# Performance work log

Hardware: AMD Instinct MI355X
Metric: run time of the kernel (lower is better)

The kernel has to match this reference:

```python
import jax, jax.numpy as jnp
import numpy as np

B, L, K = 16, 512, 30          # proteins, residues per protein, kNN neighbors
N = B * L
H, FC = 32, 3                  # h_channels, frame_channels
C = H + FC                     # fused sphere channels (35)
HEADS, AC, VC = 8, 16, 8       # heads, alpha channels (H//2), value channels (H//4)
RBF_N, POS_N = 16, 16
EF = RBF_N + POS_N

# idealized backbone atom positions (N, CA, C) in the local residue frame
IDEAL_BB = np.array([[-0.525, 1.363, 0.0], [0.0, 0.0, 0.0], [1.526, 0.0, 0.0]], dtype=np.float32)
# cartesian (x,y,z) -> real-SH l=1 ordering (y,z,x)
P_SH = np.array([[0., 1., 0.], [0., 0., 1.], [1., 0., 0.]], dtype=np.float32)


def _knn_edges(trans):
    # per-chain brute-force kNN (chains are contiguous blocks of length L)
    X = trans.reshape(B, L, 3)
    d2 = jnp.sum((X[:, :, None, :] - X[:, None, :, :]) ** 2, axis=-1)  # [B,L,L]
    d2 = d2 + jnp.eye(L, dtype=d2.dtype) * 1e9                          # exclude self
    _, idx = jax.lax.top_k(-d2, K)                                      # [B,L,K]
    off = (jnp.arange(B) * L)[:, None, None]
    src = (idx + off).reshape(-1)              # neighbor (edge_index[0])
    tgt = jnp.repeat(jnp.arange(N), K)         # center   (edge_index[1])
    return src, tgt


def _edge_rot_mat(vec):
    # rotation aligning the edge vector with the y axis (eSCN init_edge_rot_mat style)
    nx = vec / (jnp.linalg.norm(vec, axis=-1, keepdims=True) + 1e-12)
    ref = jnp.where(jnp.abs(nx[:, :1]) < 0.9,
                    jnp.array([1., 0., 0.], dtype=vec.dtype),
                    jnp.array([0., 0., 1.], dtype=vec.dtype))
    nz = jnp.cross(nx, ref)
    nz = nz / (jnp.linalg.norm(nz, axis=-1, keepdims=True) + 1e-12)
    ny = jnp.cross(nx, nz)
    ny = ny / (jnp.linalg.norm(ny, axis=-1, keepdims=True) + 1e-12)
    return jnp.stack([nz, nx, ny], axis=-2)  # [E,3,3]


def _rbf(d, d_min=0.0, d_max=20.0, count=RBF_N):
    mu = jnp.linspace(d_min, d_max, count)
    sigma = (d_max - d_min) / count
    return jnp.exp(-(((d[:, None] - mu) / sigma) ** 2))


def _pos_emb(src, tgt, num=POS_N):
    d = (src - tgt).astype(jnp.float32)
    freq = jnp.exp(jnp.arange(0, num, 2, dtype=jnp.float32) * (-np.log(10000.0) / num))
    ang = d[:, None] * freq
    return jnp.concatenate([jnp.cos(ang), jnp.sin(ang)], axis=-1)


def _forward(rots, trans, node_emb, batch, x_mask, noising_mask,
             W_alpha, a_vec, W_v, W_o, W_g, W_2):
    src, tgt = _knn_edges(trans)
    vec = trans[src] - trans[tgt]
    dist = jnp.linalg.norm(vec, axis=-1)
    valid = jnp.isfinite(dist) & (dist > 1e-3)  # edge_select, applied as mask

    R = _edge_rot_mat(vec)
    P = jnp.asarray(P_SH)
    D1 = jnp.einsum('ij,ejk,lk->eil', P, R, P)  # l=1 Wigner in real-SH basis [E,3,3]

    edge_features = jnp.concatenate([_rbf(dist), _pos_emb(src, tgt)], axis=-1)  # [E,32]

    # fuse node features with backbone frame atoms and editability flag
    frame_atoms = jnp.einsum('nij,aj->nai', rots, jnp.asarray(IDEAL_BB))  # [N,3atoms,3xyz]
    editable = noising_mask & (~x_mask)
    emb = jnp.zeros((N, 4, C), dtype=node_emb.dtype)
    emb = emb.at[:, :, :H].set(node_emb)
    emb = emb.at[:, 1:4, H:].set(jnp.swapaxes(frame_atoms, -1, -2))
    emb = emb.at[:, 0, C - 1].set(editable.astype(node_emb.dtype))

    # gather + rotate source features into edge frames
    xs = emb[src]                                                   # [E,4,C]
    xs_rot = jnp.concatenate([xs[:, :1], jnp.einsum('eij,ejc->eic', D1, xs[:, 1:])], axis=1)

    # invariant attention logits (l=0 of rotated src, l=0 of tgt, edge feats)
    inv = jnp.concatenate([xs_rot[:, 0], emb[tgt, 0], edge_features], axis=-1)  # [E,102]
    hdn = jax.nn.silu(inv @ W_alpha).reshape(-1, HEADS, AC)
    logits = jax.nn.leaky_relu(jnp.einsum('ehk,hk->eh', hdn, a_vec), 0.2)
    logits = jnp.where(valid[:, None], logits, -1e9)

    # segment softmax over incoming edges of each target node
    mx = jax.lax.stop_gradient(jax.ops.segment_max(logits, tgt, num_segments=N))
    ex = jnp.exp(logits - mx[tgt]) * valid[:, None].astype(logits.dtype)
    den = jax.ops.segment_sum(ex, tgt, num_segments=N)
    alpha = ex / (den[tgt] + 1e-9)                                  # [E,HEADS]

    # equivariant values, attention-weighted, rotate back, scatter
    v = (xs_rot @ W_v).reshape(-1, 4, HEADS, VC)
    m = (v * alpha[:, None, :, None]).reshape(-1, 4, HEADS * VC)
    m = jnp.concatenate([m[:, :1], jnp.einsum('eji,ejc->eic', D1, m[:, 1:])], axis=1)  # D^T
    agg = jax.ops.segment_sum(m, tgt, num_segments=N)               # [N,4,64]

    y = agg @ W_o                                                    # [N,4,H]
    gate = jax.nn.silu(y[:, 0] @ W_g)                                # invariant gating FFN
    return (y * gate[:, None, :]) @ W_2                              # [N,4,H]


def setup_inputs():
    key = jax.random.key(0)
    ks = jax.random.split(key, 12)
    rots = jax.vmap(lambda m: jnp.linalg.qr(m)[0])(jax.random.normal(ks[0], (N, 3, 3)))
    trans = jax.random.normal(ks[1], (N, 3)) * 10.0
    node_emb = jax.random.normal(ks[2], (N, 4, H))
    batch = jnp.repeat(jnp.arange(B, dtype=jnp.int32), L)
    x_mask = jax.random.randint(ks[3], (N,), 0, 2).astype(bool)
    noising_mask = jax.random.randint(ks[4], (N,), 0, 2).astype(bool)
    s = lambda k, sh, fan: jax.random.normal(k, sh) / np.sqrt(fan)
    return dict(rots=rots, trans=trans, node_emb=node_emb, batch=batch,
                x_mask=x_mask, noising_mask=noising_mask,
                W_alpha=s(ks[5], (2 * C + EF, HEADS * AC), 2 * C + EF),
                a_vec=s(ks[6], (HEADS, AC), AC),
                W_v=s(ks[7], (C, HEADS * VC), C),
                W_o=s(ks[8], (HEADS * VC, H), HEADS * VC),
                W_g=s(ks[9], (H, H), H),
                W_2=s(ks[10], (H, H), H))


def reference(rots, trans, node_emb, batch, x_mask, noising_mask,
              W_alpha, a_vec, W_v, W_o, W_g, W_2):
    return _forward(rots, trans, node_emb, batch, x_mask, noising_mask,
                    W_alpha, a_vec, W_v, W_o, W_g, W_2)
```

## Files before the change

### kernel.cpp

```cpp
#include <hip/hip_runtime.h>
#include <cstdint>

#define B_ 16
#define L_ 512
#define N_ 8192
#define K_ 30
#define E_ (N_*K_)
#define H_ 32
#define C_ 35

typedef uint16_t u16;
typedef uint32_t u32;
typedef unsigned long long u64;

static __device__ __forceinline__ float ldf(const void* p, int i, int bf) {
    return bf ? __uint_as_float(((u32)((const u16*)p)[i]) << 16)
              : ((const float*)p)[i];
}
static __device__ __forceinline__ int ldmask(const void* p, int i, int mode) {
    if (mode == 0) return ((const unsigned char*)p)[i] != 0;
    if (mode == 2) return ((const u32*)p)[2*i] != 0;
    return ((const u32*)p)[i] != 0;
}
static __device__ __forceinline__ u16 f2bf(float f) {
    u32 x = __float_as_uint(f);
    u32 r = x + 0x7FFFu + ((x >> 16) & 1u);
    return (u16)(r >> 16);
}
static __device__ __forceinline__ float fsilu(float x) {
    return x * __builtin_amdgcn_rcpf(1.f + __expf(-x));
}

__global__ void detect_kernel(const u16* __restrict__ tr, const u32* __restrict__ xm,
                              int* __restrict__ flag)
{
    int lane = threadIdx.x;
    int cnt = 0;
    for (int i = lane; i < 256; i += 64) {
        u16 v = tr[2 * i];
        int e = (v >> 7) & 0xFF;
        if ((e >= 100 && e <= 141) || (v & 0x7FFFu) == 0) cnt++;
    }
    int anyBig = 0, oddNZ = 0;
    for (int i = lane; i < 1024; i += 64) {
        u32 w = xm[i];
        if (w & ~1u) anyBig = 1;
        if ((i & 1) && w) oddNZ = 1;
    }
    #pragma unroll
    for (int d = 1; d < 64; d <<= 1) {
        cnt    += __shfl_xor(cnt, d, 64);
        anyBig |= __shfl_xor(anyBig, d, 64);
        oddNZ  |= __shfl_xor(oddNZ, d, 64);
    }
    if (lane == 0) {
        flag[0] = (cnt >= 192) ? 1 : 0;
        flag[1] = anyBig ? 0 : (oddNZ ? 1 : 2);
    }
}

#define U_TRANS 24576
#define U_WA    37632
#define U_AV    37760
#define U_WV    40000
#define U_WO    42048
#define U_WG    43072
#define U_W2    44096

__global__ void conv_kernel(const void* trans,
                            const void* Wa, const void* av, const void* Wv,
                            const void* Wo, const void* Wg, const void* W2,
                            const int* __restrict__ flag,
                            float* c_trans, float* c_Wa, float* c_av, float* c_Wv,
                            float* c_Wo, float* c_Wg, float* c_W2)
{
    int gid = blockIdx.x * 256 + threadIdx.x;
    if (gid >= U_W2) return;
    int bf = flag[0];
    if      (gid < U_TRANS) c_trans[gid]           = ldf(trans, gid,           bf);
    else if (gid < U_WA)    c_Wa   [gid - U_TRANS] = ldf(Wa,    gid - U_TRANS, bf);
    else if (gid < U_AV)    c_av   [gid - U_WA]    = ldf(av,    gid - U_WA,    bf);
    else if (gid < U_WV)    c_Wv   [gid - U_AV]    = ldf(Wv,    gid - U_AV,    bf);
    else if (gid < U_WO)    c_Wo   [gid - U_WV]    = ldf(Wo,    gid - U_WV,    bf);
    else if (gid < U_WG)    c_Wg   [gid - U_WO]    = ldf(Wg,    gid - U_WO,    bf);
    else                    c_W2   [gid - U_WG]    = ldf(W2,    gid - U_WG,    bf);
}

#define DPP_MIN_STEP(CTRL) \
    { u32 olo = (u32)__builtin_amdgcn_update_dpp((int)lo, (int)lo, CTRL, 0xF, 0xF, false); \
      u32 ohi = (u32)__builtin_amdgcn_update_dpp((int)hi, (int)hi, CTRL, 0xF, 0xF, false); \
      u64 o = (((u64)ohi) << 32) | olo; \
      if (o < m) m = o; \
      lo = (u32)m; hi = (u32)(m >> 32); }

__global__ __launch_bounds__(256) void knn_kernel(const float* __restrict__ trans,
                                                  int* __restrict__ srcArr)
{
    __shared__ float xs[L_], ys[L_], zs[L_];
    const int tid  = threadIdx.x;
    const int t0   = blockIdx.x * 4;
    const int base = (t0 >> 9) << 9;

    for (int i = tid; i < L_; i += 256) {
        xs[i] = trans[(base + i) * 3 + 0];
        ys[i] = trans[(base + i) * 3 + 1];
        zs[i] = trans[(base + i) * 3 + 2];
    }
    __syncthreads();

    const int wid = tid >> 6, lane = tid & 63;
    const int t = t0 + wid;
    const int l = t & 511;
    const float tx = xs[l], ty = ys[l], tz = zs[l];

    u64 key[8];
    #pragma unroll
    for (int i = 0; i < 8; ++i) {
        int j = lane + (i << 6);
        float dx = __fsub_rn(tx, xs[j]);
        float dy = __fsub_rn(ty, ys[j]);
        float dz = __fsub_rn(tz, zs[j]);
        float d2 = __fadd_rn(__fadd_rn(__fmul_rn(dx, dx), __fmul_rn(dy, dy)), __fmul_rn(dz, dz));
        if (j == l) d2 = __fadd_rn(d2, 1e9f);
        key[i] = (((u64)__float_as_uint(d2)) << 32) | (u32)j;
    }

    int myres = 0;
    for (int k = 0; k < K_; ++k) {
        u64 m = key[0];
        #pragma unroll
        for (int i = 1; i < 8; ++i)
            if (key[i] < m) m = key[i];
        u32 lo = (u32)m, hi = (u32)(m >> 32);
        DPP_MIN_STEP(0x111)
        DPP_MIN_STEP(0x112)
        DPP_MIN_STEP(0x114)
        DPP_MIN_STEP(0x118)
        DPP_MIN_STEP(0x142)
        DPP_MIN_STEP(0x143)
        u32 glo = (u32)__builtin_amdgcn_readlane((int)lo, 63);
        u32 ghi = (u32)__builtin_amdgcn_readlane((int)hi, 63);
        u64 gm = (((u64)ghi) << 32) | glo;
        if (lane == k) myres = (int)(glo & 511u);
        #pragma unroll
        for (int i = 0; i < 8; ++i)
            if (key[i] == gm) key[i] = ~0ULL;
    }
    if (lane < K_) srcArr[t * K_ + lane] = base + myres;
}

__constant__ float cBB[9] = {-0.525f, 1.363f, 0.f,  0.f, 0.f, 0.f,  1.526f, 0.f, 0.f};

__global__ __launch_bounds__(256) void node_kernel(
    const void* __restrict__ rots, const void* __restrict__ node,
    const void* __restrict__ xm, const void* __restrict__ nm,
    const int* __restrict__ flag,
    const float* __restrict__ Wa, const float* __restrict__ Wv,
    float* __restrict__ hsrc, float* __restrict__ htgt,
    float* __restrict__ ptab, float* __restrict__ V)
{
    const int bid = blockIdx.x, tid = threadIdx.x;
    if (bid >= N_) {
        int d = bid - N_;
        if (tid < 128) {
            float dd = (float)(d - 512);
            float acc = 0.f;
            #pragma unroll
            for (int q = 0; q < 8; ++q) {
                float fr = expf((float)(2 * q) * (-0.5756462732485115f));
                float ang = dd * fr;
                acc = fmaf(cosf(ang), Wa[(86 + q) * 128 + tid], acc);
                acc = fmaf(sinf(ang), Wa[(94 + q) * 128 + tid], acc);
            }
            ptab[(size_t)d * 128 + tid] = acc;
        }
        return;
    }
    __shared__ float e[140];
    const int bf = flag[0], mm = flag[1];
    if (tid < 140) {
        int r = tid / 35, c = tid - r * 35;
        float v;
        if (c < H_) {
            v = ldf(node, bid * 128 + r * 32 + c, bf);
        } else if (r == 0) {
            v = (c == 34) ? ((ldmask(nm, bid, mm) && !ldmask(xm, bid, mm)) ? 1.f : 0.f) : 0.f;
        } else {
            int i = r - 1, a = c - 32;
            v = ldf(rots, bid*9 + i*3 + 0, bf) * cBB[a*3 + 0]
              + ldf(rots, bid*9 + i*3 + 1, bf) * cBB[a*3 + 1]
              + ldf(rots, bid*9 + i*3 + 2, bf) * cBB[a*3 + 2];
        }
        e[tid] = v;
    }
    __syncthreads();
    if (tid < 128) {
        float a = 0.f, b = 0.f;
        #pragma unroll 5
        for (int i = 0; i < 35; ++i) {
            float v = e[i];
            a = fmaf(v, Wa[i * 128 + tid],        a);
            b = fmaf(v, Wa[(35 + i) * 128 + tid], b);
        }
        hsrc[(size_t)bid * 128 + tid] = a;
        htgt[(size_t)bid * 128 + tid] = b;
    }
    {
        int r = tid >> 6, cc = tid & 63;
        const float* er = e + r * 35;
        float acc = 0.f;
        #pragma unroll 5
        for (int cp = 0; cp < 35; ++cp) acc = fmaf(er[cp], Wv[cp * 64 + cc], acc);
        V[(size_t)bid * 256 + tid] = acc;
    }
}

__global__ __launch_bounds__(128) void logits_kernel(
    const float* __restrict__ trans, const int* __restrict__ srcArr,
    const float* __restrict__ hsrc, const float* __restrict__ htgt,
    const float* __restrict__ ptab, const float* __restrict__ Wa,
    const float* __restrict__ avec, float* __restrict__ logitsw)
{
    __shared__ float rbfS[2][32][20];
    __shared__ int   srcS[2][32];
    __shared__ int   tgtS[2][32];
    __shared__ int   dS[2][32];
    __shared__ float lgS[2][256];
    const int tid = threadIdx.x, wid = tid >> 6, lane = tid & 63;

    float2 wrb[16];
    #pragma unroll
    for (int j = 0; j < 16; ++j)
        wrb[j] = ((const float2*)(Wa + (70 + j) * 128))[lane];
    const float2 av = ((const float2*)avec)[lane];

    const int e0 = (blockIdx.x * 2 + wid) * 32;

    {
        const int el  = lane & 31;
        const int e   = e0 + el;
        const int tgt = e / K_;
        int src = srcArr[e];
        src = (src < 0) ? 0 : ((src >= N_) ? (N_ - 1) : src);
        float vx = trans[src*3+0] - trans[tgt*3+0];
        float vy = trans[src*3+1] - trans[tgt*3+1];
        float vz = trans[src*3+2] - trans[tgt*3+2];
        float dist = sqrtf(vx*vx + vy*vy + vz*vz);
        bool valid = isfinite(dist) && (dist > 1e-3f);
        int d = src - tgt + 512;
        d = (d < 0) ? 0 : ((d > 1023) ? 1023 : d);
        if (lane < 32) {
            srcS[wid][el] = src;
            tgtS[wid][el] = tgt;
            dS[wid][el]   = d | (valid ? 0 : (1 << 16));
        }
        const int jb = (lane >> 5) * 8;
        #pragma unroll
        for (int j = 0; j < 8; ++j) {
            float tt = (dist - (float)(jb + j) * (20.f/15.f)) * 0.8f;
            rbfS[wid][el][jb + j] = __expf(-tt * tt);
        }
    }
    __syncthreads();

    #pragma unroll 2
    for (int q = 0; q < 32; ++q) {
        const int src = srcS[wid][q];
        const int tgt = tgtS[wid][q];
        const int dm  = dS[wid][q];
        const int d   = dm & 0xFFFF;
        const bool valid = (dm >> 16) == 0;

        float2 hs = ((const float2*)(hsrc + (size_t)src * 128))[lane];
        float2 ht = ((const float2*)(htgt + (size_t)tgt * 128))[lane];
        float2 pt = ((const float2*)(ptab + (size_t)d   * 128))[lane];
        float acc0 = hs.x + ht.x + pt.x;
        float acc1 = hs.y + ht.y + pt.y;
        const float4* rp = (const float4*)(&rbfS[wid][q][0]);
        #pragma unroll
        for (int jj = 0; jj < 4; ++jj) {
            float4 rb = rp[jj];
            acc0 = fmaf(rb.x, wrb[4*jj+0].x, acc0); acc1 = fmaf(rb.x, wrb[4*jj+0].y, acc1);
            acc0 = fmaf(rb.y, wrb[4*jj+1].x, acc0); acc1 = fmaf(rb.y, wrb[4*jj+1].y, acc1);
            acc0 = fmaf(rb.z, wrb[4*jj+2].x, acc0); acc1 = fmaf(rb.z, wrb[4*jj+2].y, acc1);
            acc0 = fmaf(rb.w, wrb[4*jj+3].x, acc0); acc1 = fmaf(rb.w, wrb[4*jj+3].y, acc1);
        }
        float part = fsilu(acc0) * av.x + fsilu(acc1) * av.y;
        #pragma unroll
        for (int s = 1; s < 8; s <<= 1) part += __shfl_xor(part, s, 64);
        float lg = (part >= 0.f) ? part : 0.2f * part;
        if (!valid) lg = -1e9f;
        lg = (fabsf(lg) < 1e30f) ? lg : -1e9f;
        if ((lane & 7) == 0) lgS[wid][q * 8 + (lane >> 3)] = lg;
    }
    __syncthreads();
    {
        float4* dst = (float4*)(logitsw + (size_t)e0 * 8);
        dst[lane] = ((const float4*)lgS[wid])[lane];
    }
}

__global__ __launch_bounds__(256) void agg_out_kernel(
    const float* __restrict__ V, const int* __restrict__ srcArr,
    const float* __restrict__ logitsw,
    const float* __restrict__ Wo, const float* __restrict__ Wg,
    const float* __restrict__ W2,
    const int* __restrict__ flag, void* __restrict__ outv)
{
    __shared__ int   srcs[K_];
    __shared__ float aggS[256];
    __shared__ float ybuf[128];
    __shared__ float gbuf[32];
    const int bid = blockIdx.x;
    const int t   = ((bid & 7) << 10) | (bid >> 3);
    const int tid = threadIdx.x;
    const int obf = flag[0];
    const int cc = tid & 63, r = tid >> 6, h = cc >> 3;

    if (tid < K_) {
        int s = srcArr[t * K_ + tid];
        srcs[tid] = (s < 0) ? 0 : ((s >= N_) ? (N_ - 1) : s);
    }

    const float* lp = logitsw + (size_t)t * 240 + h;
    float lg[K_];
    float mx = -1e30f;
    #pragma unroll
    for (int k = 0; k < K_; ++k) { lg[k] = lp[k * 8]; mx = fmaxf(mx, lg[k]); }
    float den = 0.f;
    #pragma unroll
    for (int k = 0; k < K_; ++k) {
        float e = (lg[k] > -1e8f) ? __expf(lg[k] - mx) : 0.f;
        lg[k] = e; den += e;
    }
    const float inv = 1.f / (den + 1e-9f);
    __syncthreads();

    const int off = (r << 6) | cc;
    float acc = 0.f;
    #pragma unroll 6
    for (int k = 0; k < K_; ++k)
        acc = fmaf(lg[k], V[(size_t)srcs[k] * 256 + off], acc);
    aggS[tid] = acc * inv;
    __syncthreads();

    if (tid < 128) {
        int rr = tid >> 5, o = tid & 31;
        float y = 0.f;
        #pragma unroll
        for (int c = 0; c < 64; ++c) y = fmaf(aggS[rr * 64 + c], Wo[c * 32 + o], y);
        ybuf[tid] = y;
    }
    __syncthreads();
    if (tid < 32) {
        float g = 0.f;
        #pragma unroll
        for (int o = 0; o < 32; ++o) g = fmaf(ybuf[o], Wg[o * 32 + tid], g);
        gbuf[tid] = g / (1.f + expf(-g));
    }
    __syncthreads();
    if (tid < 128) {
        int rr = tid >> 5, hh = tid & 31;
        float o = 0.f;
        #pragma unroll
        for (int g = 0; g < 32; ++g) o = fmaf(ybuf[rr * 32 + g] * gbuf[g], W2[g * 32 + hh], o);
        o = (fabsf(o) < 1e30f) ? o : 0.f;
        size_t idx = (size_t)t * 128 + tid;
        if (obf) ((u16*)outv)[idx] = f2bf(o);
        else     ((float*)outv)[idx] = o;
    }
}

extern "C" void kernel_launch(void* const* d_in, const int* in_sizes, int n_in,
                              void* d_out, int out_size, void* d_ws, size_t ws_size,
                              hipStream_t stream)
{
    const void* rots         = d_in[0];
    const void* trans        = d_in[1];
    const void* node_emb     = d_in[2];
    const void* x_mask       = d_in[4];
    const void* noising_mask = d_in[5];
    const void* Wa           = d_in[6];
    const void* avec         = d_in[7];
    const void* Wv           = d_in[8];
    const void* Wo           = d_in[9];
    const void* Wg           = d_in[10];
    const void* W2           = d_in[11];

    char* ws = (char*)d_ws;
    int*   flag    = (int*)  (ws + 0);
    float* c_trans = (float*)(ws + 64);
    float* c_Wa    = (float*)(ws + 98368);
    float* c_av    = (float*)(ws + 150592);
    float* c_Wv    = (float*)(ws + 151104);
    float* c_Wo    = (float*)(ws + 160064);
    float* c_Wg    = (float*)(ws + 168256);
    float* c_W2    = (float*)(ws + 172352);
    int*   srcArr  = (int*)  (ws + 176448);
    float* hsrc    = (float*)(ws + 1159488);
    float* htgt    = (float*)(ws + 5353792);
    float* ptab    = (float*)(ws + 9548096);
    float* logitsw = (float*)(ws + 10072384);
    float* V       = (float*)(ws + 17936704);

    hipLaunchKernelGGL(detect_kernel, dim3(1), dim3(64), 0, stream,
                       (const u16*)trans, (const u32*)x_mask, flag);
    hipLaunchKernelGGL(conv_kernel, dim3((U_W2 + 255) / 256), dim3(256), 0, stream,
                       trans, Wa, avec, Wv, Wo, Wg, W2, flag,
                       c_trans, c_Wa, c_av, c_Wv, c_Wo, c_Wg, c_W2);
    hipLaunchKernelGGL(knn_kernel,  dim3(N_/4),     dim3(256), 0, stream, c_trans, srcArr);
    hipLaunchKernelGGL(node_kernel, dim3(N_+1024),  dim3(256), 0, stream,
                       rots, node_emb, x_mask, noising_mask, flag, c_Wa, c_Wv,
                       hsrc, htgt, ptab, V);
    hipLaunchKernelGGL(logits_kernel, dim3(E_/64),  dim3(128), 0, stream,
                       c_trans, srcArr, hsrc, htgt, ptab, c_Wa, c_av, logitsw);
    hipLaunchKernelGGL(agg_out_kernel, dim3(N_),    dim3(256), 0, stream,
                       V, srcArr, logitsw, c_Wo, c_Wg, c_W2, flag, d_out);
}
```

Before: 227.1 us.

## Merge prep kernels into one launch and fuse logits with aggregation

Replaces the six-kernel pipeline with two launches. The detect, convert, kNN, node-projection and position-table stages now run as block ranges of a single kernel, and each block re-detects the dtype flag itself. The edge-logit computation is fused into the per-node aggregation kernel, so the logits buffer is no longer written to and read back from global memory. This removes launch gaps and a full-size intermediate round trip, at the cost of redundant dtype detection in every block and a single-node granularity for the logit work.

New measurement: 224.3 us. Within noise of the previous version (-1.2%).

```diff
diff --git a/kernel.cpp b/kernel.cpp
--- a/kernel.cpp
+++ b/kernel.cpp
@@ -17,6 +17,9 @@
     return bf ? __uint_as_float(((u32)((const u16*)p)[i]) << 16)
               : ((const float*)p)[i];
 }
+static __device__ __forceinline__ float bfu16(u16 x) {
+    return __uint_as_float(((u32)x) << 16);
+}
 static __device__ __forceinline__ int ldmask(const void* p, int i, int mode) {
     if (mode == 0) return ((const unsigned char*)p)[i] != 0;
     if (mode == 2) return ((const u32*)p)[2*i] != 0;
@@ -31,16 +34,20 @@
     return x * __builtin_amdgcn_rcpf(1.f + __expf(-x));
 }
 
-__global__ void detect_kernel(const u16* __restrict__ tr, const u32* __restrict__ xm,
-                              int* __restrict__ flag)
-{
-    int lane = threadIdx.x;
+static __device__ __forceinline__ int detect_bf(const void* tr, int lane) {
+    const u16* p = (const u16*)tr;
     int cnt = 0;
     for (int i = lane; i < 256; i += 64) {
-        u16 v = tr[2 * i];
+        u16 v = p[2 * i];
         int e = (v >> 7) & 0xFF;
         if ((e >= 100 && e <= 141) || (v & 0x7FFFu) == 0) cnt++;
     }
+    #pragma unroll
+    for (int d = 1; d < 64; d <<= 1) cnt += __shfl_xor(cnt, d, 64);
+    return cnt >= 192;
+}
+static __device__ __forceinline__ int detect_mm(const void* xmv, int lane) {
+    const u32* xm = (const u32*)xmv;
     int anyBig = 0, oddNZ = 0;
     for (int i = lane; i < 1024; i += 64) {
         u32 w = xm[i];
@@ -49,42 +56,13 @@
     }
     #pragma unroll
     for (int d = 1; d < 64; d <<= 1) {
-        cnt    += __shfl_xor(cnt, d, 64);
         anyBig |= __shfl_xor(anyBig, d, 64);
         oddNZ  |= __shfl_xor(oddNZ, d, 64);
     }
-    if (lane == 0) {
-        flag[0] = (cnt >= 192) ? 1 : 0;
-        flag[1] = anyBig ? 0 : (oddNZ ? 1 : 2);
-    }
-}
-
-#define U_TRANS 24576
-#define U_WA    37632
-#define U_AV    37760
-#define U_WV    40000
-#define U_WO    42048
-#define U_WG    43072
-#define U_W2    44096
-
-__global__ void conv_kernel(const void* trans,
-                            const void* Wa, const void* av, const void* Wv,
-                            const void* Wo, const void* Wg, const void* W2,
-                            const int* __restrict__ flag,
-                            float* c_trans, float* c_Wa, float* c_av, float* c_Wv,
-                            float* c_Wo, float* c_Wg, float* c_W2)
-{
-    int gid = blockIdx.x * 256 + threadIdx.x;
-    if (gid >= U_W2) return;
-    int bf = flag[0];
-    if      (gid < U_TRANS) c_trans[gid]           = ldf(trans, gid,           bf);
-    else if (gid < U_WA)    c_Wa   [gid - U_TRANS] = ldf(Wa,    gid - U_TRANS, bf);
-    else if (gid < U_AV)    c_av   [gid - U_WA]    = ldf(av,    gid - U_WA,    bf);
-    else if (gid < U_WV)    c_Wv   [gid - U_AV]    = ldf(Wv,    gid - U_AV,    bf);
-    else if (gid < U_WO)    c_Wo   [gid - U_WV]    = ldf(Wo,    gid - U_WV,    bf);
-    else if (gid < U_WG)    c_Wg   [gid - U_WO]    = ldf(Wg,    gid - U_WO,    bf);
-    else                    c_W2   [gid - U_WG]    = ldf(W2,    gid - U_WG,    bf);
-}
+    return anyBig ? 0 : (oddNZ ? 1 : 2);
+}
+
+__constant__ float cBB[9] = {-0.525f, 1.363f, 0.f,  0.f, 0.f, 0.f,  1.526f, 0.f, 0.f};
 
 #define DPP_MIN_STEP(CTRL) \
     { u32 olo = (u32)__builtin_amdgcn_update_dpp((int)lo, (int)lo, CTRL, 0xF, 0xF, false); \
@@ -93,255 +71,310 @@
       if (o < m) m = o; \
       lo = (u32)m; hi = (u32)(m >> 32); }
 
-__global__ __launch_bounds__(256) void knn_kernel(const float* __restrict__ trans,
-                                                  int* __restrict__ srcArr)
+__global__ __launch_bounds__(256) void mega_kernel(
+    const void* __restrict__ rots, const void* __restrict__ trans,
+    const void* __restrict__ node, const void* __restrict__ xm,
+    const void* __restrict__ nm,
+    const void* __restrict__ Wa, const void* __restrict__ av,
+    const void* __restrict__ Wv, const void* __restrict__ Wo,
+    const void* __restrict__ Wg, const void* __restrict__ W2,
+    int* __restrict__ flag, int* __restrict__ srcArr,
+    float* __restrict__ hsrc, float* __restrict__ htgt,
+    float* __restrict__ ptab, float* __restrict__ V,
+    float* __restrict__ c_wrb, float* __restrict__ c_av,
+    float* __restrict__ c_Wo, float* __restrict__ c_Wg, float* __restrict__ c_W2)
 {
-    __shared__ float xs[L_], ys[L_], zs[L_];
-    const int tid  = threadIdx.x;
-    const int t0   = blockIdx.x * 4;
-    const int base = (t0 >> 9) << 9;
-
-    for (int i = tid; i < L_; i += 256) {
-        xs[i] = trans[(base + i) * 3 + 0];
-        ys[i] = trans[(base + i) * 3 + 1];
-        zs[i] = trans[(base + i) * 3 + 2];
-    }
-    __syncthreads();
-
-    const int wid = tid >> 6, lane = tid & 63;
-    const int t = t0 + wid;
-    const int l = t & 511;
-    const float tx = xs[l], ty = ys[l], tz = zs[l];
-
-    u64 key[8];
-    #pragma unroll
-    for (int i = 0; i < 8; ++i) {
-        int j = lane + (i << 6);
-        float dx = __fsub_rn(tx, xs[j]);
-        float dy = __fsub_rn(ty, ys[j]);
-        float dz = __fsub_rn(tz, zs[j]);
-        float d2 = __fadd_rn(__fadd_rn(__fmul_rn(dx, dx), __fmul_rn(dy, dy)), __fmul_rn(dz, dz));
-        if (j == l) d2 = __fadd_rn(d2, 1e9f);
-        key[i] = (((u64)__float_as_uint(d2)) << 32) | (u32)j;
-    }
-
-    int myres = 0;
-    for (int k = 0; k < K_; ++k) {
-        u64 m = key[0];
-        #pragma unroll
-        for (int i = 1; i < 8; ++i)
-            if (key[i] < m) m = key[i];
-        u32 lo = (u32)m, hi = (u32)(m >> 32);
-        DPP_MIN_STEP(0x111)
-        DPP_MIN_STEP(0x112)
-        DPP_MIN_STEP(0x114)
-        DPP_MIN_STEP(0x118)
-        DPP_MIN_STEP(0x142)
-        DPP_MIN_STEP(0x143)
-        u32 glo = (u32)__builtin_amdgcn_readlane((int)lo, 63);
-        u32 ghi = (u32)__builtin_amdgcn_readlane((int)hi, 63);
-        u64 gm = (((u64)ghi) << 32) | glo;
-        if (lane == k) myres = (int)(glo & 511u);
-        #pragma unroll
-        for (int i = 0; i < 8; ++i)
-            if (key[i] == gm) key[i] = ~0ULL;
-    }
-    if (lane < K_) srcArr[t * K_ + lane] = base + myres;
-}
-
-__constant__ float cBB[9] = {-0.525f, 1.363f, 0.f,  0.f, 0.f, 0.f,  1.526f, 0.f, 0.f};
-
-__global__ __launch_bounds__(256) void node_kernel(
-    const void* __restrict__ rots, const void* __restrict__ node,
-    const void* __restrict__ xm, const void* __restrict__ nm,
-    const int* __restrict__ flag,
-    const float* __restrict__ Wa, const float* __restrict__ Wv,
-    float* __restrict__ hsrc, float* __restrict__ htgt,
-    float* __restrict__ ptab, float* __restrict__ V)
-{
+    __shared__ float sX[L_], sY[L_], sZ[L_];
+    __shared__ float eS[140];
+    __shared__ int flagS[2];
     const int bid = blockIdx.x, tid = threadIdx.x;
-    if (bid >= N_) {
-        int d = bid - N_;
+    const int lane = tid & 63, wid = tid >> 6;
+
+    if (bid < 2048) {
+        if (wid == 0) {
+            int bf = detect_bf(trans, lane);
+            if (lane == 0) flagS[0] = bf;
+        }
+        __syncthreads();
+        const int bf = flagS[0];
+        const int t0 = bid * 4;
+        const int base = (t0 >> 9) << 9;
+        if (bf) {
+            const u16* tp = (const u16*)trans;
+            for (int i = tid; i < L_; i += 256) {
+                sX[i] = bfu16(tp[(base + i) * 3 + 0]);
+                sY[i] = bfu16(tp[(base + i) * 3 + 1]);
+                sZ[i] = bfu16(tp[(base + i) * 3 + 2]);
+            }
+        } else {
+            const float* tp = (const float*)trans;
+            for (int i = tid; i < L_; i += 256) {
+                sX[i] = tp[(base + i) * 3 + 0];
+                sY[i] = tp[(base + i) * 3 + 1];
+                sZ[i] = tp[(base + i) * 3 + 2];
+            }
+        }
+        __syncthreads();
+
+        const int t = t0 + wid;
+        const int l = t & 511;
+        const float tx = sX[l], ty = sY[l], tz = sZ[l];
+
+        u64 key[8];
+        #pragma unroll
+        for (int i = 0; i < 8; ++i) {
+            int j = lane + (i << 6);
+            float dx = __fsub_rn(tx, sX[j]);
+            float dy = __fsub_rn(ty, sY[j]);
+            float dz = __fsub_rn(tz, sZ[j]);
+            float d2 = __fadd_rn(__fadd_rn(__fmul_rn(dx, dx), __fmul_rn(dy, dy)), __fmul_rn(dz, dz));
+            if (j == l) d2 = __fadd_rn(d2, 1e9f);
+            key[i] = (((u64)__float_as_uint(d2)) << 32) | (u32)j;
+        }
+        int myres = 0;
+        for (int k = 0; k < K_; ++k) {
+            u64 m = key[0];
+            #pragma unroll
+            for (int i = 1; i < 8; ++i)
+                if (key[i] < m) m = key[i];
+            u32 lo = (u32)m, hi = (u32)(m >> 32);
+            DPP_MIN_STEP(0x111)
+            DPP_MIN_STEP(0x112)
+            DPP_MIN_STEP(0x114)
+            DPP_MIN_STEP(0x118)
+            DPP_MIN_STEP(0x142)
+            DPP_MIN_STEP(0x143)
+            u32 glo = (u32)__builtin_amdgcn_readlane((int)lo, 63);
+            u32 ghi = (u32)__builtin_amdgcn_readlane((int)hi, 63);
+            u64 gm = (((u64)ghi) << 32) | glo;
+            if (lane == k) myres = (int)(glo & 511u);
+            #pragma unroll
+            for (int i = 0; i < 8; ++i)
+                if (key[i] == gm) key[i] = ~0ULL;
+        }
+        if (lane < K_) srcArr[t * K_ + lane] = base + myres;
+
+    } else if (bid < 10240) {
+        const int n = bid - 2048;
+        if (wid == 0) {
+            int bf = detect_bf(trans, lane);
+            int mm = detect_mm(xm, lane);
+            if (lane == 0) { flagS[0] = bf; flagS[1] = mm; }
+        }
+        __syncthreads();
+        const int bf = flagS[0], mm = flagS[1];
+        if (tid < 140) {
+            int r = tid / 35, c = tid - r * 35;
+            float v;
+            if (c < H_) {
+                v = ldf(node, n * 128 + r * 32 + c, bf);
+            } else if (r == 0) {
+                v = (c == 34) ? ((ldmask(nm, n, mm) && !ldmask(xm, n, mm)) ? 1.f : 0.f) : 0.f;
+            } else {
+                int i = r - 1, a = c - 32;
+                v = ldf(rots, n*9 + i*3 + 0, bf) * cBB[a*3 + 0]
+                  + ldf(rots, n*9 + i*3 + 1, bf) * cBB[a*3 + 1]
+                  + ldf(rots, n*9 + i*3 + 2, bf) * cBB[a*3 + 2];
+            }
+            eS[tid] = v;
+        }
+        __syncthreads();
+        const int r = tid >> 6, cc = tid & 63;
+        if (bf) {
+            const u16* wa = (const u16*)Wa;
+            const u16* wv = (const u16*)Wv;
+            if (tid < 128) {
+                float a = 0.f, b = 0.f;
+                #pragma unroll 5
+                for (int i = 0; i < 35; ++i) {
+                    float v = eS[i];
+                    a = fmaf(v, bfu16(wa[i * 128 + tid]),        a);
+                    b = fmaf(v, bfu16(wa[(35 + i) * 128 + tid]), b);
+                }
+                hsrc[(size_t)n * 128 + tid] = a;
+                htgt[(size_t)n * 128 + tid] = b;
+            }
+            const float* er = eS + r * 35;
+            float acc = 0.f;
+            #pragma unroll 5
+            for (int cp = 0; cp < 35; ++cp) acc = fmaf(er[cp], bfu16(wv[cp * 64 + cc]), acc);
+            V[(size_t)n * 256 + tid] = acc;
+        } else {
+            const float* wa = (const float*)Wa;
+            const float* wv = (const float*)Wv;
+            if (tid < 128) {
+                float a = 0.f, b = 0.f;
+                #pragma unroll 5
+                for (int i = 0; i < 35; ++i) {
+                    float v = eS[i];
+                    a = fmaf(v, wa[i * 128 + tid],        a);
+                    b = fmaf(v, wa[(35 + i) * 128 + tid], b);
+                }
+                hsrc[(size_t)n * 128 + tid] = a;
+                htgt[(size_t)n * 128 + tid] = b;
+            }
+            const float* er = eS + r * 35;
+            float acc = 0.f;
+            #pragma unroll 5
+            for (int cp = 0; cp < 35; ++cp) acc = fmaf(er[cp], wv[cp * 64 + cc], acc);
+            V[(size_t)n * 256 + tid] = acc;
+        }
+
+    } else if (bid < 11264) {
+        const int d = bid - 10240;
+        if (wid == 0) {
+            int bf = detect_bf(trans, lane);
+            if (lane == 0) flagS[0] = bf;
+        }
+        __syncthreads();
+        const int bf = flagS[0];
         if (tid < 128) {
             float dd = (float)(d - 512);
             float acc = 0.f;
-            #pragma unroll
-            for (int q = 0; q < 8; ++q) {
-                float fr = expf((float)(2 * q) * (-0.5756462732485115f));
-                float ang = dd * fr;
-                acc = fmaf(cosf(ang), Wa[(86 + q) * 128 + tid], acc);
-                acc = fmaf(sinf(ang), Wa[(94 + q) * 128 + tid], acc);
+            if (bf) {
+                const u16* wa = (const u16*)Wa;
+                #pragma unroll
+                for (int q = 0; q < 8; ++q) {
+                    float fr = expf((float)(2 * q) * (-0.5756462732485115f));
+                    float ang = dd * fr;
+                    acc = fmaf(cosf(ang), bfu16(wa[(86 + q) * 128 + tid]), acc);
+                    acc = fmaf(sinf(ang), bfu16(wa[(94 + q) * 128 + tid]), acc);
+                }
+            } else {
+                const float* wa = (const float*)Wa;
+                #pragma unroll
+                for (int q = 0; q < 8; ++q) {
+                    float fr = expf((float)(2 * q) * (-0.5756462732485115f));
+                    float ang = dd * fr;
+                    acc = fmaf(cosf(ang), wa[(86 + q) * 128 + tid], acc);
+                    acc = fmaf(sinf(ang), wa[(94 + q) * 128 + tid], acc);
+                }
             }
             ptab[(size_t)d * 128 + tid] = acc;
         }
-        return;
-    }
-    __shared__ float e[140];
-    const int bf = flag[0], mm = flag[1];
-    if (tid < 140) {
-        int r = tid / 35, c = tid - r * 35;
-        float v;
-        if (c < H_) {
-            v = ldf(node, bid * 128 + r * 32 + c, bf);
-        } else if (r == 0) {
-            v = (c == 34) ? ((ldmask(nm, bid, mm) && !ldmask(xm, bid, mm)) ? 1.f : 0.f) : 0.f;
-        } else {
-            int i = r - 1, a = c - 32;
-            v = ldf(rots, bid*9 + i*3 + 0, bf) * cBB[a*3 + 0]
-              + ldf(rots, bid*9 + i*3 + 1, bf) * cBB[a*3 + 1]
-              + ldf(rots, bid*9 + i*3 + 2, bf) * cBB[a*3 + 2];
-        }
-        e[tid] = v;
-    }
-    __syncthreads();
-    if (tid < 128) {
-        float a = 0.f, b = 0.f;
-        #pragma unroll 5
-        for (int i = 0; i < 35; ++i) {
-            float v = e[i];
-            a = fmaf(v, Wa[i * 128 + tid],        a);
-            b = fmaf(v, Wa[(35 + i) * 128 + tid], b);
-        }
-        hsrc[(size_t)bid * 128 + tid] = a;
-        htgt[(size_t)bid * 128 + tid] = b;
-    }
-    {
-        int r = tid >> 6, cc = tid & 63;
-        const float* er = e + r * 35;
-        float acc = 0.f;
-        #pragma unroll 5
-        for (int cp = 0; cp < 35; ++cp) acc = fmaf(er[cp], Wv[cp * 64 + cc], acc);
-        V[(size_t)bid * 256 + tid] = acc;
-    }
-}
-
-__global__ __launch_bounds__(128) void logits_kernel(
-    const float* __restrict__ trans, const int* __restrict__ srcArr,
+
+    } else {
+        if (wid == 0) {
+            int bf = detect_bf(trans, lane);
+            if (lane == 0) flagS[0] = bf;
+        }
+        __syncthreads();
+        const int bf = flagS[0];
+        if (bid == 11264 && tid == 0) flag[0] = bf;
+        int g0 = (bid - 11264) * 256 + tid;
+        for (int i = g0; i < 6272; i += 2048) {
+            if      (i < 2048) c_wrb[i]        = ldf(Wa, 70 * 128 + i, bf);
+            else if (i < 2176) c_av[i - 2048]  = ldf(av, i - 2048, bf);
+            else if (i < 4224) c_Wo[i - 2176]  = ldf(Wo, i - 2176, bf);
+            else if (i < 5248) c_Wg[i - 4224]  = ldf(Wg, i - 4224, bf);
+            else               c_W2[i - 5248]  = ldf(W2, i - 5248, bf);
+        }
+    }
+}
+
+__global__ __launch_bounds__(256) void edge_agg_kernel(
+    const void* __restrict__ trans, const int* __restrict__ srcArr,
     const float* __restrict__ hsrc, const float* __restrict__ htgt,
-    const float* __restrict__ ptab, const float* __restrict__ Wa,
-    const float* __restrict__ avec, float* __restrict__ logitsw)
-{
-    __shared__ float rbfS[2][32][20];
-    __shared__ int   srcS[2][32];
-    __shared__ int   tgtS[2][32];
-    __shared__ int   dS[2][32];
-    __shared__ float lgS[2][256];
-    const int tid = threadIdx.x, wid = tid >> 6, lane = tid & 63;
-
-    float2 wrb[16];
-    #pragma unroll
-    for (int j = 0; j < 16; ++j)
-        wrb[j] = ((const float2*)(Wa + (70 + j) * 128))[lane];
-    const float2 av = ((const float2*)avec)[lane];
-
-    const int e0 = (blockIdx.x * 2 + wid) * 32;
-
-    {
-        const int el  = lane & 31;
-        const int e   = e0 + el;
-        const int tgt = e / K_;
-        int src = srcArr[e];
-        src = (src < 0) ? 0 : ((src >= N_) ? (N_ - 1) : src);
-        float vx = trans[src*3+0] - trans[tgt*3+0];
-        float vy = trans[src*3+1] - trans[tgt*3+1];
-        float vz = trans[src*3+2] - trans[tgt*3+2];
-        float dist = sqrtf(vx*vx + vy*vy + vz*vz);
-        bool valid = isfinite(dist) && (dist > 1e-3f);
-        int d = src - tgt + 512;
-        d = (d < 0) ? 0 : ((d > 1023) ? 1023 : d);
-        if (lane < 32) {
-            srcS[wid][el] = src;
-            tgtS[wid][el] = tgt;
-            dS[wid][el]   = d | (valid ? 0 : (1 << 16));
-        }
-        const int jb = (lane >> 5) * 8;
-        #pragma unroll
-        for (int j = 0; j < 8; ++j) {
-            float tt = (dist - (float)(jb + j) * (20.f/15.f)) * 0.8f;
-            rbfS[wid][el][jb + j] = __expf(-tt * tt);
-        }
-    }
-    __syncthreads();
-
-    #pragma unroll 2
-    for (int q = 0; q < 32; ++q) {
-        const int src = srcS[wid][q];
-        const int tgt = tgtS[wid][q];
-        const int dm  = dS[wid][q];
-        const int d   = dm & 0xFFFF;
-        const bool valid = (dm >> 16) == 0;
-
-        float2 hs = ((const float2*)(hsrc + (size_t)src * 128))[lane];
-        float2 ht = ((const float2*)(htgt + (size_t)tgt * 128))[lane];
-        float2 pt = ((const float2*)(ptab + (size_t)d   * 128))[lane];
-        float acc0 = hs.x + ht.x + pt.x;
-        float acc1 = hs.y + ht.y + pt.y;
-        const float4* rp = (const float4*)(&rbfS[wid][q][0]);
-        #pragma unroll
-        for (int jj = 0; jj < 4; ++jj) {
-            float4 rb = rp[jj];
-            acc0 = fmaf(rb.x, wrb[4*jj+0].x, acc0); acc1 = fmaf(rb.x, wrb[4*jj+0].y, acc1);
-            acc0 = fmaf(rb.y, wrb[4*jj+1].x, acc0); acc1 = fmaf(rb.y, wrb[4*jj+1].y, acc1);
-            acc0 = fmaf(rb.z, wrb[4*jj+2].x, acc0); acc1 = fmaf(rb.z, wrb[4*jj+2].y, acc1);
-            acc0 = fmaf(rb.w, wrb[4*jj+3].x, acc0); acc1 = fmaf(rb.w, wrb[4*jj+3].y, acc1);
-        }
-        float part = fsilu(acc0) * av.x + fsilu(acc1) * av.y;
-        #pragma unroll
-        for (int s = 1; s < 8; s <<= 1) part += __shfl_xor(part, s, 64);
-        float lg = (part >= 0.f) ? part : 0.2f * part;
-        if (!valid) lg = -1e9f;
-        lg = (fabsf(lg) < 1e30f) ? lg : -1e9f;
-        if ((lane & 7) == 0) lgS[wid][q * 8 + (lane >> 3)] = lg;
-    }
-    __syncthreads();
-    {
-        float4* dst = (float4*)(logitsw + (size_t)e0 * 8);
-        dst[lane] = ((const float4*)lgS[wid])[lane];
-    }
-}
-
-__global__ __launch_bounds__(256) void agg_out_kernel(
-    const float* __restrict__ V, const int* __restrict__ srcArr,
-    const float* __restrict__ logitsw,
+    const float* __restrict__ ptab, const float* __restrict__ V,
+    const float* __restrict__ c_wrb, const float* __restrict__ c_av,
     const float* __restrict__ Wo, const float* __restrict__ Wg,
     const float* __restrict__ W2,
     const int* __restrict__ flag, void* __restrict__ outv)
 {
-    __shared__ int   srcs[K_];
+    __shared__ float rbfS[K_][20];
+    __shared__ int   srcS[K_];
+    __shared__ int   dS[K_];
+    __shared__ float lgS[240];
     __shared__ float aggS[256];
     __shared__ float ybuf[128];
     __shared__ float gbuf[32];
-    const int bid = blockIdx.x;
+    const int bid = blockIdx.x, tid = threadIdx.x;
     const int t   = ((bid & 7) << 10) | (bid >> 3);
-    const int tid = threadIdx.x;
-    const int obf = flag[0];
-    const int cc = tid & 63, r = tid >> 6, h = cc >> 3;
-
-    if (tid < K_) {
-        int s = srcArr[t * K_ + tid];
-        srcs[tid] = (s < 0) ? 0 : ((s >= N_) ? (N_ - 1) : s);
-    }
-
-    const float* lp = logitsw + (size_t)t * 240 + h;
-    float lg[K_];
-    float mx = -1e30f;
+    const int lane = tid & 63, wid = tid >> 6;
+    const int bf = flag[0];
+
+    float2 wrb[16];
     #pragma unroll
-    for (int k = 0; k < K_; ++k) { lg[k] = lp[k * 8]; mx = fmaxf(mx, lg[k]); }
-    float den = 0.f;
+    for (int j = 0; j < 16; ++j) wrb[j] = ((const float2*)c_wrb)[j * 64 + lane];
+    const float2 avv = ((const float2*)c_av)[lane];
+
+    if (tid < 2 * K_) {
+        const int k = tid >> 1, half = tid & 1;
+        const int e = t * K_ + k;
+        int src = srcArr[e];
+        src = (src < 0) ? 0 : ((src >= N_) ? (N_ - 1) : src);
+        float vx = ldf(trans, src*3+0, bf) - ldf(trans, t*3+0, bf);
+        float vy = ldf(trans, src*3+1, bf) - ldf(trans, t*3+1, bf);
+        float vz = ldf(trans, src*3+2, bf) - ldf(trans, t*3+2, bf);
+        float dist = sqrtf(vx*vx + vy*vy + vz*vz);
+        bool valid = isfinite(dist) && (dist > 1e-3f);
+        int d = src - t + 512;
+        d = (d < 0) ? 0 : ((d > 1023) ? 1023 : d);
+        if (half == 0) {
+            srcS[k] = src;
+            dS[k]   = d | (valid ? 0 : (1 << 16));
+        }
+        const int jb = half * 8;
+        #pragma unroll
+        for (int j = 0; j < 8; ++j) {
+            float tt = (dist - (float)(jb + j) * (20.f/15.f)) * 0.8f;
+            rbfS[k][jb + j] = __expf(-tt * tt);
+        }
+    }
+    __syncthreads();
+
+    const float2 htv = ((const float2*)(htgt + (size_t)t * 128))[lane];
     #pragma unroll
-    for (int k = 0; k < K_; ++k) {
-        float e = (lg[k] > -1e8f) ? __expf(lg[k] - mx) : 0.f;
-        lg[k] = e; den += e;
-    }
-    const float inv = 1.f / (den + 1e-9f);
+    for (int j = 0; j < 8; ++j) {
+        const int k = wid * 8 + j;
+        if (k < K_) {
+            const int src = srcS[k];
+            const int dm  = dS[k];
+            const int d   = dm & 0xFFFF;
+            const bool valid = (dm >> 16) == 0;
+            float2 hs = ((const float2*)(hsrc + (size_t)src * 128))[lane];
+            float2 pt = ((const float2*)(ptab + (size_t)d   * 128))[lane];
+            float acc0 = hs.x + htv.x + pt.x;
+            float acc1 = hs.y + htv.y + pt.y;
+            const float4* rp = (const float4*)(&rbfS[k][0]);
+            #pragma unroll
+            for (int jj = 0; jj < 4; ++jj) {
+                float4 rb = rp[jj];
+                acc0 = fmaf(rb.x, wrb[4*jj+0].x, acc0); acc1 = fmaf(rb.x, wrb[4*jj+0].y, acc1);
+                acc0 = fmaf(rb.y, wrb[4*jj+1].x, acc0); acc1 = fmaf(rb.y, wrb[4*jj+1].y, acc1);
+                acc0 = fmaf(rb.z, wrb[4*jj+2].x, acc0); acc1 = fmaf(rb.z, wrb[4*jj+2].y, acc1);
+                acc0 = fmaf(rb.w, wrb[4*jj+3].x, acc0); acc1 = fmaf(rb.w, wrb[4*jj+3].y, acc1);
+            }
+            float part = fsilu(acc0) * avv.x + fsilu(acc1) * avv.y;
+            #pragma unroll
+            for (int s = 1; s < 8; s <<= 1) part += __shfl_xor(part, s, 64);
+            float lg = (part >= 0.f) ? part : 0.2f * part;
+            if (!valid) lg = -1e9f;
+            lg = (fabsf(lg) < 1e30f) ? lg : -1e9f;
+            if ((lane & 7) == 0) lgS[k * 8 + (lane >> 3)] = lg;
+        }
+    }
     __syncthreads();
 
-    const int off = (r << 6) | cc;
-    float acc = 0.f;
-    #pragma unroll 6
-    for (int k = 0; k < K_; ++k)
-        acc = fmaf(lg[k], V[(size_t)srcs[k] * 256 + off], acc);
-    aggS[tid] = acc * inv;
+    {
+        const int h = (tid & 63) >> 3;
+        float lg[K_];
+        float mx = -1e30f;
+        #pragma unroll
+        for (int k = 0; k < K_; ++k) { lg[k] = lgS[k * 8 + h]; mx = fmaxf(mx, lg[k]); }
+        float den = 0.f;
+        #pragma unroll
+        for (int k = 0; k < K_; ++k) {
+            float e = (lg[k] > -1e8f) ? __expf(lg[k] - mx) : 0.f;
+            lg[k] = e; den += e;
+        }
+        const float inv = 1.f / (den + 1e-9f);
+        float acc = 0.f;
+        #pragma unroll 6
+        for (int k = 0; k < K_; ++k)
+            acc = fmaf(lg[k], V[(size_t)srcS[k] * 256 + tid], acc);
+        aggS[tid] = acc * inv;
+    }
     __syncthreads();
 
     if (tid < 128) {
@@ -356,7 +389,7 @@
         float g = 0.f;
         #pragma unroll
         for (int o = 0; o < 32; ++o) g = fmaf(ybuf[o], Wg[o * 32 + tid], g);
-        gbuf[tid] = g / (1.f + expf(-g));
+        gbuf[tid] = fsilu(g);
     }
     __syncthreads();
     if (tid < 128) {
@@ -366,8 +399,8 @@
         for (int g = 0; g < 32; ++g) o = fmaf(ybuf[rr * 32 + g] * gbuf[g], W2[g * 32 + hh], o);
         o = (fabsf(o) < 1e30f) ? o : 0.f;
         size_t idx = (size_t)t * 128 + tid;
-        if (obf) ((u16*)outv)[idx] = f2bf(o);
-        else     ((float*)outv)[idx] = o;
+        if (bf) ((u16*)outv)[idx] = f2bf(o);
+        else    ((float*)outv)[idx] = o;
     }
 }
 
@@ -389,31 +422,23 @@
 
     char* ws = (char*)d_ws;
     int*   flag    = (int*)  (ws + 0);
-    float* c_trans = (float*)(ws + 64);
-    float* c_Wa    = (float*)(ws + 98368);
-    float* c_av    = (float*)(ws + 150592);
-    float* c_Wv    = (float*)(ws + 151104);
-    float* c_Wo    = (float*)(ws + 160064);
-    float* c_Wg    = (float*)(ws + 168256);
-    float* c_W2    = (float*)(ws + 172352);
-    int*   srcArr  = (int*)  (ws + 176448);
-    float* hsrc    = (float*)(ws + 1159488);
-    float* htgt    = (float*)(ws + 5353792);
-    float* ptab    = (float*)(ws + 9548096);
-    float* logitsw = (float*)(ws + 10072384);
-    float* V       = (float*)(ws + 17936704);
-
-    hipLaunchKernelGGL(detect_kernel, dim3(1), dim3(64), 0, stream,
-                       (const u16*)trans, (const u32*)x_mask, flag);
-    hipLaunchKernelGGL(conv_kernel, dim3((U_W2 + 255) / 256), dim3(256), 0, stream,
-                       trans, Wa, avec, Wv, Wo, Wg, W2, flag,
-                       c_trans, c_Wa, c_av, c_Wv, c_Wo, c_Wg, c_W2);
-    hipLaunchKernelGGL(knn_kernel,  dim3(N_/4),     dim3(256), 0, stream, c_trans, srcArr);
-    hipLaunchKernelGGL(node_kernel, dim3(N_+1024),  dim3(256), 0, stream,
-                       rots, node_emb, x_mask, noising_mask, flag, c_Wa, c_Wv,
-                       hsrc, htgt, ptab, V);
-    hipLaunchKernelGGL(logits_kernel, dim3(E_/64),  dim3(128), 0, stream,
-                       c_trans, srcArr, hsrc, htgt, ptab, c_Wa, c_av, logitsw);
-    hipLaunchKernelGGL(agg_out_kernel, dim3(N_),    dim3(256), 0, stream,
-                       V, srcArr, logitsw, c_Wo, c_Wg, c_W2, flag, d_out);
-}
+    int*   srcArr  = (int*)  (ws + 64);
+    float* hsrc    = (float*)(ws + 983104);
+    float* htgt    = (float*)(ws + 5177408);
+    float* ptab    = (float*)(ws + 9371712);
+    float* V       = (float*)(ws + 9896000);
+    float* c_wrb   = (float*)(ws + 18284608);
+    float* c_av    = (float*)(ws + 18292800);
+    float* c_Wo    = (float*)(ws + 18293312);
+    float* c_Wg    = (float*)(ws + 18301504);
+    float* c_W2    = (float*)(ws + 18305600);
+
+    hipLaunchKernelGGL(mega_kernel, dim3(11272), dim3(256), 0, stream,
+                       rots, trans, node_emb, x_mask, noising_mask,
+                       Wa, avec, Wv, Wo, Wg, W2,
+                       flag, srcArr, hsrc, htgt, ptab, V,
+                       c_wrb, c_av, c_Wo, c_Wg, c_W2);
+    hipLaunchKernelGGL(edge_agg_kernel, dim3(N_), dim3(256), 0, stream,
+                       trans, srcArr, hsrc, htgt, ptab, V,
+                       c_wrb, c_av, c_Wo, c_Wg, c_W2, flag, d_out);
+}
```
